# Kernel optimization log

Hardware: AMD Instinct MI355X
Metric: run time of the kernel (lower is better)

Reference implementation:

```python
import jax, jax.numpy as jnp
import numpy as np
from jax.scipy.special import logsumexp

PAD = 0  # NlpContext().padding_idx


def setup_inputs() -> dict:
    key = jax.random.key(0)
    k1, k2, k3 = jax.random.split(key, 3)
    B, S, L = 4, 1024, 128
    pred = jax.random.normal(k1, (B, S, L), dtype=jnp.float32)
    # labels in [1, L): no token equals PAD -> mask is all-zero, non_pad_length == S
    gt = jax.random.randint(k2, (B, S), 1, L)
    transition = jax.random.normal(k3, (L, L), dtype=jnp.float32)
    return {"pred": pred, "gt": gt, "transition": transition}


def _crf_loss(pred, gt, transition):
    # Faithful translation of LinearCRFLoss.forward (including the alpha
    # broadcasting behaviour of the original torch loop).
    mask = (gt == PAD).astype(pred.dtype)                 # (B,S), all-zero here
    logp = jax.nn.log_softmax(pred, -1) * (1.0 - mask)[:, :, None]  # (B,S,L)
    trans = jax.nn.log_softmax(transition, -1)            # (L,L)

    # posterior_t[b,i,j] = log_softmax_j( logp[b,t,i] + trans[i,j]*(1-mask[b,t]) )
    post = jax.nn.log_softmax(
        logp[:, :, :, None] + trans[None, None] * (1.0 - mask)[:, :, None, None],
        axis=-1,
    )  # (B,S,L,L)

    # t = 1: alpha has shape (B,L,1) in the original -> broadcasts over 'to'
    # axis j; reduce (logsumexp) over the 'from' axis i.
    alpha = logsumexp(post[:, 1] + logp[:, 0, :, None], axis=1)  # (B,L)
    # t >= 2: alpha has shape (B,1,L) in the original -> broadcasts over the
    # 'from' axis i, so it factors out of the logsumexp:
    #   alpha_t[j] = alpha_{t-1}[j] + lse_i post_t[i,j]
    # which telescopes into a single sum over t (identical math, vectorized).
    alpha = alpha + logsumexp(post[:, 2:], axis=2).sum(axis=1)   # (B,L)
    forward_score = logsumexp(alpha, axis=-1)                    # (B,)

    # gold path score (non_pad_length == S since there is no padding)
    emit = jnp.take_along_axis(logp, gt[:, :, None], axis=2)[..., 0].sum(-1)  # (B,)
    tr = trans[gt[:, :-1], gt[:, 1:]].sum(-1)                                  # (B,)
    gold = emit + tr
    return -(gold - forward_score).mean()


def reference(pred, gt, transition):
    return _crf_loss(pred, gt, transition)
```

## Files before the change

### kernel.cpp

```cpp
#include <hip/hip_runtime.h>
#include <hip/hip_bf16.h>
#include <math.h>

#define BB 4
#define SS 1024
#define LL 128

__global__ __launch_bounds__(256) void crf_rows_kernel(
    const float* __restrict__ pred,
    const int* __restrict__ gt,
    float* __restrict__ ws_part,
    float* __restrict__ ws_logp0)
{
    const int wave = threadIdx.x >> 6;
    const int lane = threadIdx.x & 63;
    const int row0 = blockIdx.x * 16;

    float2 v[4];
    #pragma unroll
    for (int it = 0; it < 4; ++it) {
        const int r = row0 + it * 4 + wave;
        v[it] = ((const float2*)(pred + (size_t)r * LL))[lane];
    }
    float gval[4] = {0.f, 0.f, 0.f, 0.f};
    if (lane == 0) {
        int gi[4];
        #pragma unroll
        for (int it = 0; it < 4; ++it) gi[it] = gt[row0 + it * 4 + wave];
        #pragma unroll
        for (int it = 0; it < 4; ++it)
            gval[it] = pred[(size_t)(row0 + it * 4 + wave) * LL + gi[it]];
    }

    float local = 0.f;
    #pragma unroll
    for (int it = 0; it < 4; ++it) {
        float m = fmaxf(v[it].x, v[it].y);
        #pragma unroll
        for (int off = 32; off > 0; off >>= 1) m = fmaxf(m, __shfl_xor(m, off));
        float s = __expf(v[it].x - m) + __expf(v[it].y - m);
        #pragma unroll
        for (int off = 32; off > 0; off >>= 1) s += __shfl_xor(s, off);
        const float lse = m + __logf(s);

        if (lane == 0) local += gval[it] - lse;

        if (it == 0 && wave == 0 && (blockIdx.x & 63) == 0) {
            const int b = blockIdx.x >> 6;
            ws_logp0[b * LL + 2 * lane]     = v[0].x - lse;
            ws_logp0[b * LL + 2 * lane + 1] = v[0].y - lse;
        }
    }

    __shared__ float red[4];
    if (lane == 0) red[wave] = local;
    __syncthreads();
    if (threadIdx.x == 0)
        ws_part[blockIdx.x] = red[0] + red[1] + red[2] + red[3];
}

__global__ __launch_bounds__(512) void crf_finish_kernel(
    const float* __restrict__ transition,
    const int* __restrict__ gt,
    const float* __restrict__ ws_part,
    const float* __restrict__ ws_logp0,
    float* __restrict__ out)
{
    __shared__ float tr_s[LL][LL + 1];
    __shared__ float logp0_s[BB][LL];
    __shared__ float redm[4][LL];
    __shared__ float reds[4][LL];
    __shared__ float lse_s[LL];
    __shared__ float c_s[LL];
    __shared__ float emit_s[BB];
    __shared__ float gold_s[BB];
    __shared__ float wred[16];

    const int tid  = threadIdx.x;
    const int lane = tid & 63;
    const int wave = tid >> 6;

    for (int idx = tid; idx < LL * LL; idx += 512)
        tr_s[idx >> 7][idx & (LL - 1)] = transition[idx];
    if (tid < BB * LL)
        logp0_s[tid >> 7][tid & (LL - 1)] = ws_logp0[tid];
    if (wave < BB) {
        float p = ws_part[wave * 64 + lane];
        #pragma unroll
        for (int off = 32; off > 0; off >>= 1) p += __shfl_xor(p, off);
        if (lane == 0) emit_s[wave] = p;
    }
    __syncthreads();

    const int sub = tid >> 7;
    const int rc  = tid & 127;
    {
        const float* rp = &tr_s[rc][sub * 32];
        float m = -INFINITY;
        #pragma unroll
        for (int k = 0; k < 32; ++k) m = fmaxf(m, rp[k]);
        float s = 0.f;
        #pragma unroll
        for (int k = 0; k < 32; ++k) s += __expf(rp[k] - m);
        redm[sub][rc] = m;
        reds[sub][rc] = s;
    }
    __syncthreads();
    if (tid < LL) {
        float m0 = redm[0][tid], m1 = redm[1][tid], m2 = redm[2][tid], m3 = redm[3][tid];
        float mm = fmaxf(fmaxf(m0, m1), fmaxf(m2, m3));
        float ss = reds[0][tid] * __expf(m0 - mm) + reds[1][tid] * __expf(m1 - mm)
                 + reds[2][tid] * __expf(m2 - mm) + reds[3][tid] * __expf(m3 - mm);
        lse_s[tid] = mm + __logf(ss);
    }
    __syncthreads();
    {
        const float l = lse_s[rc];
        float* wp = &tr_s[rc][sub * 32];
        #pragma unroll
        for (int k = 0; k < 32; ++k) wp[k] -= l;
    }
    __syncthreads();

    {
        float m = -INFINITY;
        #pragma unroll
        for (int k = 0; k < 32; ++k) m = fmaxf(m, tr_s[sub * 32 + k][rc]);
        float s = 0.f;
        #pragma unroll
        for (int k = 0; k < 32; ++k) s += __expf(tr_s[sub * 32 + k][rc] - m);
        redm[sub][rc] = m;
        reds[sub][rc] = s;
    }
    {
        const int b  = tid >> 7;
        const int t0 = tid & 127;
        const int* gtb = gt + b * SS;
        float g = 0.f;
        for (int t = t0; t < SS - 1; t += 128)
            g += tr_s[gtb[t]][gtb[t + 1]];
        #pragma unroll
        for (int off = 32; off > 0; off >>= 1) g += __shfl_xor(g, off);
        if (lane == 0) wred[wave] = g;
    }
    __syncthreads();
    if (tid < LL) {
        float m0 = redm[0][tid], m1 = redm[1][tid], m2 = redm[2][tid], m3 = redm[3][tid];
        float mm = fmaxf(fmaxf(m0, m1), fmaxf(m2, m3));
        float ss = reds[0][tid] * __expf(m0 - mm) + reds[1][tid] * __expf(m1 - mm)
                 + reds[2][tid] * __expf(m2 - mm) + reds[3][tid] * __expf(m3 - mm);
        c_s[tid] = mm + __logf(ss);
    }
    if (tid < BB)
        gold_s[tid] = wred[2 * tid] + wred[2 * tid + 1];
    __syncthreads();

    const int b = tid >> 7;
    const int j = tid & 127;
    float am = -INFINITY, as = 0.f;
    const float* lp = logp0_s[b];
    for (int i = 0; i < LL; ++i) {
        const float v  = tr_s[i][j] + lp[i];
        const float mn = fmaxf(am, v);
        as = as * __expf(am - mn) + __expf(v - mn);
        am = mn;
    }
    const float alpha = am + __logf(as) + (float)(SS - 2) * c_s[j];

    float wm = alpha;
    #pragma unroll
    for (int off = 32; off > 0; off >>= 1) wm = fmaxf(wm, __shfl_xor(wm, off));
    float wsum = __expf(alpha - wm);
    #pragma unroll
    for (int off = 32; off > 0; off >>= 1) wsum += __shfl_xor(wsum, off);
    if (lane == 0) { redm[0][wave] = wm; reds[0][wave] = wsum; }
    __syncthreads();
    if (tid < BB) {
        const float m0 = redm[0][2 * tid], m1 = redm[0][2 * tid + 1];
        const float mm = fmaxf(m0, m1);
        const float ss = reds[0][2 * tid] * __expf(m0 - mm)
                       + reds[0][2 * tid + 1] * __expf(m1 - mm);
        const float fwd = mm + __logf(ss);
        wred[tid] = emit_s[tid] + gold_s[tid] - fwd;
    }
    __syncthreads();
    if (tid == 0)
        out[0] = -(wred[0] + wred[1] + wred[2] + wred[3]) * (1.0f / BB);
}

extern "C" void kernel_launch(void* const* d_in, const int* in_sizes, int n_in,
                              void* d_out, int out_size, void* d_ws, size_t ws_size,
                              hipStream_t stream) {
    const float* pred       = (const float*)d_in[0];
    const int*   gt         = (const int*)d_in[1];
    const float* transition = (const float*)d_in[2];
    float* out = (float*)d_out;

    float* ws_part  = (float*)d_ws;
    float* ws_logp0 = ws_part + 256;

    crf_rows_kernel<<<(BB * SS) / 16, 256, 0, stream>>>(pred, gt, ws_part, ws_logp0);
    crf_finish_kernel<<<1, 512, 0, stream>>>(transition, gt, ws_part, ws_logp0, out);
}
```

Measured before the change: 70.73 us.

## Move transition row log-softmax into row kernel and use exp-domain sums

```diff
diff --git a/kernel.cpp b/kernel.cpp
--- a/kernel.cpp
+++ b/kernel.cpp
@@ -6,11 +6,14 @@
 #define SS 1024
 #define LL 128
 
+
 __global__ __launch_bounds__(256) void crf_rows_kernel(
     const float* __restrict__ pred,
     const int* __restrict__ gt,
+    const float* __restrict__ transition,
     float* __restrict__ ws_part,
-    float* __restrict__ ws_logp0)
+    float* __restrict__ ws_elp,
+    float* __restrict__ ws_trans)
 {
     const int wave = threadIdx.x >> 6;
     const int lane = threadIdx.x & 63;
@@ -47,9 +50,22 @@
 
         if (it == 0 && wave == 0 && (blockIdx.x & 63) == 0) {
             const int b = blockIdx.x >> 6;
-            ws_logp0[b * LL + 2 * lane]     = v[0].x - lse;
-            ws_logp0[b * LL + 2 * lane + 1] = v[0].y - lse;
+            ws_elp[b * LL + 2 * lane]     = __expf(v[0].x - lse);
+            ws_elp[b * LL + 2 * lane + 1] = __expf(v[0].y - lse);
         }
+    }
+
+    if (blockIdx.x < LL && wave == 0) {
+        const float2 tv = ((const float2*)(transition + blockIdx.x * LL))[lane];
+        float m = fmaxf(tv.x, tv.y);
+        #pragma unroll
+        for (int off = 32; off > 0; off >>= 1) m = fmaxf(m, __shfl_xor(m, off));
+        float s = __expf(tv.x - m) + __expf(tv.y - m);
+        #pragma unroll
+        for (int off = 32; off > 0; off >>= 1) s += __shfl_xor(s, off);
+        const float lse = m + __logf(s);
+        float2 o; o.x = tv.x - lse; o.y = tv.y - lse;
+        ((float2*)(ws_trans + blockIdx.x * LL))[lane] = o;
     }
 
     __shared__ float red[4];
@@ -59,31 +75,33 @@
         ws_part[blockIdx.x] = red[0] + red[1] + red[2] + red[3];
 }
 
+#define PADL (LL + 4)
 __global__ __launch_bounds__(512) void crf_finish_kernel(
-    const float* __restrict__ transition,
     const int* __restrict__ gt,
     const float* __restrict__ ws_part,
-    const float* __restrict__ ws_logp0,
+    const float* __restrict__ ws_elp,
+    const float* __restrict__ ws_trans,
     float* __restrict__ out)
 {
-    __shared__ float tr_s[LL][LL + 1];
-    __shared__ float logp0_s[BB][LL];
-    __shared__ float redm[4][LL];
-    __shared__ float reds[4][LL];
-    __shared__ float lse_s[LL];
-    __shared__ float c_s[LL];
+    __shared__ float tr_s[LL][PADL];
+    __shared__ float elp_s[BB][LL];
+    __shared__ float pc[4][LL];
+    __shared__ float pa[4][BB][LL];
     __shared__ float emit_s[BB];
-    __shared__ float gold_s[BB];
-    __shared__ float wred[16];
+    __shared__ float wred[8];
+    __shared__ float fm[8], fs[8];
 
     const int tid  = threadIdx.x;
     const int lane = tid & 63;
     const int wave = tid >> 6;
 
-    for (int idx = tid; idx < LL * LL; idx += 512)
-        tr_s[idx >> 7][idx & (LL - 1)] = transition[idx];
-    if (tid < BB * LL)
-        logp0_s[tid >> 7][tid & (LL - 1)] = ws_logp0[tid];
+    #pragma unroll
+    for (int k = 0; k < 8; ++k) {
+        const int e = (tid + k * 512) * 4;
+        const int i = e >> 7, j = e & (LL - 1);
+        *(float4*)&tr_s[i][j] = ((const float4*)ws_trans)[e >> 2];
+    }
+    elp_s[tid >> 7][tid & (LL - 1)] = ws_elp[tid];
     if (wave < BB) {
         float p = ws_part[wave * 64 + lane];
         #pragma unroll
@@ -92,100 +110,65 @@
     }
     __syncthreads();
 
-    const int sub = tid >> 7;
-    const int rc  = tid & 127;
     {
-        const float* rp = &tr_s[rc][sub * 32];
-        float m = -INFINITY;
+        const int sub = tid >> 7;
+        const int j   = tid & (LL - 1);
+        float sc = 0.f, s0 = 0.f, s1 = 0.f, s2 = 0.f, s3 = 0.f;
         #pragma unroll
-        for (int k = 0; k < 32; ++k) m = fmaxf(m, rp[k]);
-        float s = 0.f;
-        #pragma unroll
-        for (int k = 0; k < 32; ++k) s += __expf(rp[k] - m);
-        redm[sub][rc] = m;
-        reds[sub][rc] = s;
-    }
-    __syncthreads();
-    if (tid < LL) {
-        float m0 = redm[0][tid], m1 = redm[1][tid], m2 = redm[2][tid], m3 = redm[3][tid];
-        float mm = fmaxf(fmaxf(m0, m1), fmaxf(m2, m3));
-        float ss = reds[0][tid] * __expf(m0 - mm) + reds[1][tid] * __expf(m1 - mm)
-                 + reds[2][tid] * __expf(m2 - mm) + reds[3][tid] * __expf(m3 - mm);
-        lse_s[tid] = mm + __logf(ss);
-    }
-    __syncthreads();
-    {
-        const float l = lse_s[rc];
-        float* wp = &tr_s[rc][sub * 32];
-        #pragma unroll
-        for (int k = 0; k < 32; ++k) wp[k] -= l;
-    }
-    __syncthreads();
-
-    {
-        float m = -INFINITY;
-        #pragma unroll
-        for (int k = 0; k < 32; ++k) m = fmaxf(m, tr_s[sub * 32 + k][rc]);
-        float s = 0.f;
-        #pragma unroll
-        for (int k = 0; k < 32; ++k) s += __expf(tr_s[sub * 32 + k][rc] - m);
-        redm[sub][rc] = m;
-        reds[sub][rc] = s;
+        for (int k = 0; k < 32; ++k) {
+            const int i = sub * 32 + k;
+            const float e = __expf(tr_s[i][j]);
+            sc += e;
+            s0 += e * elp_s[0][i];
+            s1 += e * elp_s[1][i];
+            s2 += e * elp_s[2][i];
+            s3 += e * elp_s[3][i];
+        }
+        pc[sub][j] = sc;
+        pa[sub][0][j] = s0; pa[sub][1][j] = s1;
+        pa[sub][2][j] = s2; pa[sub][3][j] = s3;
     }
     {
         const int b  = tid >> 7;
-        const int t0 = tid & 127;
+        const int t0 = tid & (LL - 1);
         const int* gtb = gt + b * SS;
         float g = 0.f;
-        for (int t = t0; t < SS - 1; t += 128)
+        for (int t = t0; t < SS - 1; t += LL)
             g += tr_s[gtb[t]][gtb[t + 1]];
         #pragma unroll
         for (int off = 32; off > 0; off >>= 1) g += __shfl_xor(g, off);
         if (lane == 0) wred[wave] = g;
     }
     __syncthreads();
-    if (tid < LL) {
-        float m0 = redm[0][tid], m1 = redm[1][tid], m2 = redm[2][tid], m3 = redm[3][tid];
-        float mm = fmaxf(fmaxf(m0, m1), fmaxf(m2, m3));
-        float ss = reds[0][tid] * __expf(m0 - mm) + reds[1][tid] * __expf(m1 - mm)
-                 + reds[2][tid] * __expf(m2 - mm) + reds[3][tid] * __expf(m3 - mm);
-        c_s[tid] = mm + __logf(ss);
+
+    {
+        const int b = tid >> 7;
+        const int j = tid & (LL - 1);
+        const float csum = pc[0][j] + pc[1][j] + pc[2][j] + pc[3][j];
+        const float asum = pa[0][b][j] + pa[1][b][j] + pa[2][b][j] + pa[3][b][j];
+        const float alpha = __logf(asum) + (float)(SS - 2) * __logf(csum);
+
+        float wm = alpha;
+        #pragma unroll
+        for (int off = 32; off > 0; off >>= 1) wm = fmaxf(wm, __shfl_xor(wm, off));
+        float wsum = __expf(alpha - wm);
+        #pragma unroll
+        for (int off = 32; off > 0; off >>= 1) wsum += __shfl_xor(wsum, off);
+        if (lane == 0) { fm[wave] = wm; fs[wave] = wsum; }
     }
-    if (tid < BB)
-        gold_s[tid] = wred[2 * tid] + wred[2 * tid + 1];
     __syncthreads();
 
-    const int b = tid >> 7;
-    const int j = tid & 127;
-    float am = -INFINITY, as = 0.f;
-    const float* lp = logp0_s[b];
-    for (int i = 0; i < LL; ++i) {
-        const float v  = tr_s[i][j] + lp[i];
-        const float mn = fmaxf(am, v);
-        as = as * __expf(am - mn) + __expf(v - mn);
-        am = mn;
-    }
-    const float alpha = am + __logf(as) + (float)(SS - 2) * c_s[j];
-
-    float wm = alpha;
-    #pragma unroll
-    for (int off = 32; off > 0; off >>= 1) wm = fmaxf(wm, __shfl_xor(wm, off));
-    float wsum = __expf(alpha - wm);
-    #pragma unroll
-    for (int off = 32; off > 0; off >>= 1) wsum += __shfl_xor(wsum, off);
-    if (lane == 0) { redm[0][wave] = wm; reds[0][wave] = wsum; }
-    __syncthreads();
     if (tid < BB) {
-        const float m0 = redm[0][2 * tid], m1 = redm[0][2 * tid + 1];
+        const float m0 = fm[2 * tid], m1 = fm[2 * tid + 1];
         const float mm = fmaxf(m0, m1);
-        const float ss = reds[0][2 * tid] * __expf(m0 - mm)
-                       + reds[0][2 * tid + 1] * __expf(m1 - mm);
-        const float fwd = mm + __logf(ss);
-        wred[tid] = emit_s[tid] + gold_s[tid] - fwd;
+        const float fwd = mm + __logf(fs[2 * tid] * __expf(m0 - mm)
+                                    + fs[2 * tid + 1] * __expf(m1 - mm));
+        const float gold = wred[2 * tid] + wred[2 * tid + 1];
+        fm[tid] = emit_s[tid] + gold - fwd;
     }
     __syncthreads();
     if (tid == 0)
-        out[0] = -(wred[0] + wred[1] + wred[2] + wred[3]) * (1.0f / BB);
+        out[0] = -(fm[0] + fm[1] + fm[2] + fm[3]) * (1.0f / BB);
 }
 
 extern "C" void kernel_launch(void* const* d_in, const int* in_sizes, int n_in,
@@ -197,8 +180,10 @@
     float* out = (float*)d_out;
 
     float* ws_part  = (float*)d_ws;
-    float* ws_logp0 = ws_part + 256;
+    float* ws_elp   = ws_part + 256;
+    float* ws_trans = ws_part + 768;
 
-    crf_rows_kernel<<<(BB * SS) / 16, 256, 0, stream>>>(pred, gt, ws_part, ws_logp0);
-    crf_finish_kernel<<<1, 512, 0, stream>>>(transition, gt, ws_part, ws_logp0, out);
+    crf_rows_kernel<<<(BB * SS) / 16, 256, 0, stream>>>(
+        pred, gt, transition, ws_part, ws_elp, ws_trans);
+    crf_finish_kernel<<<1, 512, 0, stream>>>(gt, ws_part, ws_elp, ws_trans, out);
 }
```

Result: faster. 64.49 us (-8.8%).
